# Performance work log

Measured on AMD Instinct MI355X. Metric: run time of the kernel, lower is better.

The kernel has to match this reference:

```python
import jax, jax.numpy as jnp
import numpy as np

B, S, E, H = 4, 2048, 1024, 16
D = E // H  # head_size = 64


def setup_inputs() -> dict:
    key = jax.random.key(0)
    k1, k2 = jax.random.split(key)
    x = jax.random.normal(k1, (B, S, E), dtype=jnp.float32)
    # fused QKV projection weight (torch Linear(E, 3E, bias=False))
    W_qkv = jax.random.normal(k2, (E, 3 * E), dtype=jnp.float32) * (1.0 / np.sqrt(E))
    return {"x": x, "W_qkv": W_qkv}


def reference(x, W_qkv):
    b, s, e = x.shape
    qkv = x @ W_qkv                              # [B,S,3E]
    q, k, v = jnp.split(qkv, 3, axis=-1)
    # [B,S,E] -> [B,H,S,D]
    q = q.reshape(b, s, H, D).transpose(0, 2, 1, 3)
    k = k.reshape(b, s, H, D).transpose(0, 2, 1, 3)
    v = v.reshape(b, s, H, D).transpose(0, 2, 1, 3)
    scores = jnp.einsum("bhqd,bhkd->bhqk", q, k) * (1.0 / np.sqrt(D))
    causal = jnp.tril(jnp.ones((s, s), dtype=bool))  # [S,S]
    scores = jnp.where(causal[None, None, :, :], scores, jnp.float32(-jnp.inf))
    attn = jax.nn.softmax(scores, axis=-1)
    # dropout is identity in eval mode (p effectively 0 for this baseline)
    out = jnp.einsum("bhqk,bhkd->bhqd", attn, v)  # [B,H,S,D]
    out = out.transpose(0, 2, 1, 3).reshape(b, s, e)
    # NOTE: original forward never applies output_projection; faithful omission.
    return out
```

## Files before the change

kernel.cpp:

```cpp
#include <hip/hip_runtime.h>
#include <hip/hip_bf16.h>
#include <cstdint>
#include <cstddef>

#define GLOBAL_AS __attribute__((address_space(1)))
#define LDS_AS __attribute__((address_space(3)))

typedef short bf16x8 __attribute__((ext_vector_type(8)));
typedef float f32x4 __attribute__((ext_vector_type(4)));

constexpr int Bq = 4, Sq = 2048, Eq = 1024, Hh = 16;
constexpr int M = Bq * Sq;
constexpr int K = 1024;
constexpr int N = 3 * Eq;

#define SMSC 0.18033688f
#define SMBIAS (-16.0f)

static __device__ __forceinline__ unsigned f2bf(float f) {
    union { float f; unsigned u; } v; v.f = f;
    unsigned r = v.u + 0x7fffu + ((v.u >> 16) & 1u);
    return r >> 16;
}

static __device__ __forceinline__ unsigned pk2(float a, float b) {
    union { __hip_bfloat162 h; unsigned u; } c;
    c.h = __float22bfloat162_rn(float2{a, b});
    return c.u;
}

__global__ __launch_bounds__(256) void prep(const float* __restrict__ X,
                                            unsigned short* __restrict__ Xb,
                                            const float* __restrict__ W,
                                            unsigned short* __restrict__ Wt) {
    __shared__ unsigned short tile[64 * 72];
    const int t = threadIdx.x;
    const int bx = blockIdx.x;
    if (bx < 4096) {
        size_t i = ((size_t)bx * 256 + t) * 8;
        float4 a = *reinterpret_cast<const float4*>(X + i);
        float4 b = *reinterpret_cast<const float4*>(X + i + 4);
        uint4 o;
        o.x = pk2(a.x, a.y);
        o.y = pk2(a.z, a.w);
        o.z = pk2(b.x, b.y);
        o.w = pk2(b.z, b.w);
        *reinterpret_cast<uint4*>(Xb + i) = o;
        return;
    }
    const int idx = bx - 4096;
    const int n0 = (idx % 48) * 64;
    const int k0 = (idx / 48) * 64;
    #pragma unroll
    for (int p = 0; p < 4; ++p) {
        int c = p * 256 + t;
        int row = c >> 4;
        int c4 = (c & 15) * 4;
        float4 v = *reinterpret_cast<const float4*>(W + (size_t)(k0 + row) * N + n0 + c4);
        *reinterpret_cast<unsigned*>(&tile[row * 72 + c4]) = pk2(v.x, v.y);
        *reinterpret_cast<unsigned*>(&tile[row * 72 + c4 + 2]) = pk2(v.z, v.w);
    }
    __syncthreads();
    #pragma unroll
    for (int p = 0; p < 2; ++p) {
        int c = t + p * 256;
        int n = c & 63;
        int kc = (c >> 6) * 8;
        unsigned v[8];
        #pragma unroll
        for (int j = 0; j < 8; ++j) v[j] = tile[(kc + j) * 72 + n];
        uint4 o;
        o.x = v[0] | (v[1] << 16);
        o.y = v[2] | (v[3] << 16);
        o.z = v[4] | (v[5] << 16);
        o.w = v[6] | (v[7] << 16);
        *reinterpret_cast<uint4*>(Wt + (size_t)(n0 + n) * K + k0 + kc) = o;
    }
}

__global__ __launch_bounds__(256) void gemm_qkv(const unsigned short* __restrict__ A,
                                                const unsigned short* __restrict__ Bt,
                                                unsigned short* __restrict__ C) {
    __shared__ unsigned short Alds[128 * 64];
    __shared__ unsigned short Blds[128 * 64];
    const int t = threadIdx.x;
    const int lane = t & 63, w = t >> 6;
    const int wm = w >> 1, wn = w & 1;
    const int m0 = blockIdx.y * 128, n0 = blockIdx.x * 128;
    const int lr = lane & 15, quad = lane >> 4;
    const int sw = lr & 7;

    f32x4 acc[4][4] = {};
    for (int k0 = 0; k0 < K; k0 += 64) {
        #pragma unroll
        for (int p = 0; p < 4; ++p) {
            int c = p * 256 + t;
            int row = c >> 3;
            int lch = (c & 7) ^ (row & 7);
            const unsigned short* ga = A + (size_t)(m0 + row) * K + k0 + lch * 8;
            __builtin_amdgcn_global_load_lds((const GLOBAL_AS unsigned int*)ga,
                                             (LDS_AS unsigned int*)&Alds[c * 8], 16, 0, 0);
            const unsigned short* gb = Bt + (size_t)(n0 + row) * K + k0 + lch * 8;
            __builtin_amdgcn_global_load_lds((const GLOBAL_AS unsigned int*)gb,
                                             (LDS_AS unsigned int*)&Blds[c * 8], 16, 0, 0);
        }
        __syncthreads();
        #pragma unroll
        for (int ks = 0; ks < 2; ++ks) {
            bf16x8 af[4], bfr[4];
            const int pch = ((ks * 4 + quad) ^ sw) << 3;
            #pragma unroll
            for (int mt = 0; mt < 4; ++mt)
                af[mt] = *reinterpret_cast<const bf16x8*>(
                    &Alds[(wm * 64 + mt * 16 + lr) * 64 + pch]);
            #pragma unroll
            for (int nt = 0; nt < 4; ++nt)
                bfr[nt] = *reinterpret_cast<const bf16x8*>(
                    &Blds[(wn * 64 + nt * 16 + lr) * 64 + pch]);
            #pragma unroll
            for (int mt = 0; mt < 4; ++mt)
                #pragma unroll
                for (int nt = 0; nt < 4; ++nt)
                    acc[mt][nt] = __builtin_amdgcn_mfma_f32_16x16x32_bf16(af[mt], bfr[nt],
                                                                          acc[mt][nt], 0, 0, 0);
        }
        __syncthreads();
    }
    #pragma unroll
    for (int mt = 0; mt < 4; ++mt)
        #pragma unroll
        for (int nt = 0; nt < 4; ++nt)
            #pragma unroll
            for (int r = 0; r < 4; ++r) {
                int row = m0 + wm * 64 + mt * 16 + quad * 4 + r;
                int col = n0 + wn * 64 + nt * 16 + lr;
                C[(size_t)row * N + col] = (unsigned short)f2bf(acc[mt][nt][r]);
            }
}

__global__ __launch_bounds__(256) void transpose_v(const unsigned short* __restrict__ QKV,
                                                   unsigned short* __restrict__ Vt) {
    __shared__ unsigned short tile[64 * 72];
    const int t = threadIdx.x;
    const int s0 = blockIdx.x * 64;
    const int h = blockIdx.y, b = blockIdx.z;
    #pragma unroll
    for (int p = 0; p < 2; ++p) {
        int c = t + p * 256;
        int row = c >> 3;
        int col0 = (c & 7) * 8;
        *reinterpret_cast<uint4*>(&tile[row * 72 + col0]) =
            *reinterpret_cast<const uint4*>(QKV + (size_t)(b * Sq + s0 + row) * N + 2 * Eq + h * 64 + col0);
    }
    __syncthreads();
    #pragma unroll
    for (int p = 0; p < 2; ++p) {
        int c = t + p * 256;
        int d = c & 63;
        int sc = (c >> 6) * 8;
        unsigned v[8];
        #pragma unroll
        for (int j = 0; j < 8; ++j) v[j] = tile[(sc + j) * 72 + d];
        uint4 o;
        o.x = v[0] | (v[1] << 16);
        o.y = v[2] | (v[3] << 16);
        o.z = v[4] | (v[5] << 16);
        o.w = v[6] | (v[7] << 16);
        *reinterpret_cast<uint4*>(Vt + (size_t)((b * Hh + h) * 64 + d) * Sq + s0 + sc) = o;
    }
}

__global__ __launch_bounds__(256) void flash_attn(const unsigned short* __restrict__ QKV,
                                                  const unsigned short* __restrict__ Vt,
                                                  float* __restrict__ Out) {
    __shared__ unsigned short Klds[2][64 * 64];
    __shared__ unsigned short Vlds[2][64 * 64];
    __shared__ unsigned short Plds[4][32 * 72];
    const int t = threadIdx.x;
    const int lane = t & 63, w = t >> 6;
    const int lr = lane & 15, quad = lane >> 4;
    const int hb = blockIdx.x;
    const int h = hb & 15, b = hb >> 4;
    const int i = 15 - (int)blockIdx.y;
    const int jmax = 2 * i + 1;
    const int jd = 2 * i + (w >> 1);
    const int qbase = i * 128 + w * 32;
    unsigned short* Pl = Plds[w];
    const int sw = lr & 7;

    const unsigned short* Kbase = QKV + (size_t)b * Sq * N + Eq + h * 64;
    const unsigned short* Vbase = Vt + (size_t)((b * Hh + h) * 64) * Sq;

    bf16x8 ones;
    #pragma unroll
    for (int z = 0; z < 8; ++z) ones[z] = (short)0x3F80;

    auto stage = [&](int j, int buf) {
        const int kv0 = j * 64;
        #pragma unroll
        for (int p = 0; p < 2; ++p) {
            int c = p * 256 + t;
            int row = c >> 3;
            int lch = (c & 7) ^ (row & 7);
            const unsigned short* gk = Kbase + (size_t)(kv0 + row) * N + lch * 8;
            __builtin_amdgcn_global_load_lds((const GLOBAL_AS unsigned int*)gk,
                                             (LDS_AS unsigned int*)&Klds[buf][c * 8], 16, 0, 0);
            const unsigned short* gv = Vbase + (size_t)row * Sq + kv0 + lch * 8;
            __builtin_amdgcn_global_load_lds((const GLOBAL_AS unsigned int*)gv,
                                             (LDS_AS unsigned int*)&Vlds[buf][c * 8], 16, 0, 0);
        }
    };

    bf16x8 qf[2][2];
    #pragma unroll
    for (int mt = 0; mt < 2; ++mt)
        #pragma unroll
        for (int ks = 0; ks < 2; ++ks)
            qf[mt][ks] = *reinterpret_cast<const bf16x8*>(
                QKV + (size_t)(b * Sq + qbase + mt * 16 + lr) * N + h * 64 + ks * 32 + quad * 8);

    f32x4 o[2][4] = {};
    f32x4 lsum[2] = {};

    stage(0, 0);
    int cur = 0;
    for (int j = 0; j <= jmax; ++j) {
        __syncthreads();
        if (j < jmax) stage(j + 1, cur ^ 1);

        if (j <= jd) {
            const unsigned short* Kb = Klds[cur];
            const unsigned short* Vb = Vlds[cur];
            const int kv0 = j * 64;

            f32x4 sa[2][4] = {};
            #pragma unroll
            for (int ks = 0; ks < 2; ++ks) {
                const int pch = ((ks * 4 + quad) ^ sw) << 3;
                #pragma unroll
                for (int nt = 0; nt < 4; ++nt) {
                    bf16x8 kf = *reinterpret_cast<const bf16x8*>(&Kb[(nt * 16 + lr) * 64 + pch]);
                    #pragma unroll
                    for (int mt = 0; mt < 2; ++mt)
                        sa[mt][nt] = __builtin_amdgcn_mfma_f32_16x16x32_bf16(qf[mt][ks], kf,
                                                                             sa[mt][nt], 0, 0, 0);
                }
            }

            if (j == jd) {
                #pragma unroll
                for (int mt = 0; mt < 2; ++mt)
                    #pragma unroll
                    for (int nt = 0; nt < 4; ++nt)
                        #pragma unroll
                        for (int r = 0; r < 4; ++r) {
                            int qg = qbase + mt * 16 + quad * 4 + r;
                            int kvg = kv0 + nt * 16 + lr;
                            float sc = fmaf(sa[mt][nt][r], SMSC, SMBIAS);
                            sc = (kvg > qg) ? -1e30f : sc;
                            Pl[(mt * 16 + quad * 4 + r) * 72 + nt * 16 + lr] =
                                (unsigned short)(__float_as_uint(exp2f(sc)) >> 16);
                        }
            } else {
                #pragma unroll
                for (int mt = 0; mt < 2; ++mt)
                    #pragma unroll
                    for (int nt = 0; nt < 4; ++nt)
                        #pragma unroll
                        for (int r = 0; r < 4; ++r)
                            Pl[(mt * 16 + quad * 4 + r) * 72 + nt * 16 + lr] =
                                (unsigned short)(__float_as_uint(
                                    exp2f(fmaf(sa[mt][nt][r], SMSC, SMBIAS))) >> 16);
            }
            asm volatile("s_waitcnt lgkmcnt(0)" ::: "memory");

            bf16x8 pf[2][2];
            #pragma unroll
            for (int mt = 0; mt < 2; ++mt)
                #pragma unroll
                for (int ks = 0; ks < 2; ++ks)
                    pf[mt][ks] = *reinterpret_cast<const bf16x8*>(
                        &Pl[(mt * 16 + lr) * 72 + ks * 32 + quad * 8]);

            #pragma unroll
            for (int ks = 0; ks < 2; ++ks) {
                const int pch = ((ks * 4 + quad) ^ sw) << 3;
                #pragma unroll
                for (int dt = 0; dt < 4; ++dt) {
                    bf16x8 vf = *reinterpret_cast<const bf16x8*>(&Vb[(dt * 16 + lr) * 64 + pch]);
                    #pragma unroll
                    for (int mt = 0; mt < 2; ++mt)
                        o[mt][dt] = __builtin_amdgcn_mfma_f32_16x16x32_bf16(pf[mt][ks], vf,
                                                                            o[mt][dt], 0, 0, 0);
                }
                #pragma unroll
                for (int mt = 0; mt < 2; ++mt)
                    lsum[mt] = __builtin_amdgcn_mfma_f32_16x16x32_bf16(pf[mt][ks], ones,
                                                                       lsum[mt], 0, 0, 0);
            }
        }
        cur ^= 1;
    }

    #pragma unroll
    for (int mt = 0; mt < 2; ++mt)
        #pragma unroll
        for (int r = 0; r < 4; ++r) {
            float inv = 1.0f / lsum[mt][r];
            int qg = qbase + mt * 16 + quad * 4 + r;
            #pragma unroll
            for (int dt = 0; dt < 4; ++dt)
                Out[(size_t)(b * Sq + qg) * Eq + h * 64 + dt * 16 + lr] = o[mt][dt][r] * inv;
        }
}

extern "C" void kernel_launch(void* const* d_in, const int* in_sizes, int n_in,
                              void* d_out, int out_size, void* d_ws, size_t ws_size,
                              hipStream_t stream) {
    const float* x  = (const float*)d_in[0];
    const float* Wq = (const float*)d_in[1];
    float* out = (float*)d_out;

    unsigned short* xb  = (unsigned short*)d_ws;
    unsigned short* qkv = xb + (size_t)M * K;
    unsigned short* Wt  = qkv + (size_t)M * N;
    unsigned short* Vt  = Wt + (size_t)N * K;

    prep<<<dim3(4096 + 768), 256, 0, stream>>>(x, xb, Wq, Wt);
    gemm_qkv<<<dim3(N / 128, M / 128), 256, 0, stream>>>(xb, Wt, qkv);
    transpose_v<<<dim3(Sq / 64, Hh, Bq), 256, 0, stream>>>(qkv, Vt);
    flash_attn<<<dim3(Hh * Bq, 16), 256, 0, stream>>>(qkv, Vt, out);
}
```

Before: 249.1 us.

## Fuse V transpose into GEMM epilogue and shrink attention KV tile to 32

The QKV GEMM epilogue now writes the V columns directly in transposed [B,H,D,S] layout, which removes the separate transpose_v kernel and its extra read and write of V. The flash attention kernel moves from 64-key to 32-key tiles with smaller LDS buffers and a launch-bounds occupancy hint of 4 blocks, so causal masking wastes less work per warp (each warp stops at its own diagonal tile). The cost is more loop iterations and barriers per block, and narrower uint2 scattered stores in the GEMM epilogue.

```diff
diff --git a/kernel.cpp b/kernel.cpp
--- a/kernel.cpp
+++ b/kernel.cpp
@@ -80,7 +80,8 @@
 
 __global__ __launch_bounds__(256) void gemm_qkv(const unsigned short* __restrict__ A,
                                                 const unsigned short* __restrict__ Bt,
-                                                unsigned short* __restrict__ C) {
+                                                unsigned short* __restrict__ C,
+                                                unsigned short* __restrict__ Vt) {
     __shared__ unsigned short Alds[128 * 64];
     __shared__ unsigned short Blds[128 * 64];
     const int t = threadIdx.x;
@@ -126,64 +127,49 @@
         }
         __syncthreads();
     }
-    #pragma unroll
-    for (int mt = 0; mt < 4; ++mt)
-        #pragma unroll
-        for (int nt = 0; nt < 4; ++nt)
-            #pragma unroll
-            for (int r = 0; r < 4; ++r) {
-                int row = m0 + wm * 64 + mt * 16 + quad * 4 + r;
-                int col = n0 + wn * 64 + nt * 16 + lr;
-                C[(size_t)row * N + col] = (unsigned short)f2bf(acc[mt][nt][r]);
+    if (n0 < 2 * Eq) {
+        #pragma unroll
+        for (int mt = 0; mt < 4; ++mt)
+            #pragma unroll
+            for (int nt = 0; nt < 4; ++nt)
+                #pragma unroll
+                for (int r = 0; r < 4; ++r) {
+                    int row = m0 + wm * 64 + mt * 16 + quad * 4 + r;
+                    int col = n0 + wn * 64 + nt * 16 + lr;
+                    C[(size_t)row * N + col] = (unsigned short)f2bf(acc[mt][nt][r]);
+                }
+    } else {
+        const int b2 = m0 >> 11;
+        const int sbase = (m0 & 2047) + wm * 64;
+        #pragma unroll
+        for (int mt = 0; mt < 4; ++mt)
+            #pragma unroll
+            for (int nt = 0; nt < 4; ++nt) {
+                int hd = n0 - 2 * Eq + wn * 64 + nt * 16 + lr;
+                size_t rowV = (size_t)(b2 * Hh + (hd >> 6)) * 64 + (hd & 63);
+                int s = sbase + mt * 16 + quad * 4;
+                uint2 val;
+                val.x = f2bf(acc[mt][nt][0]) | (f2bf(acc[mt][nt][1]) << 16);
+                val.y = f2bf(acc[mt][nt][2]) | (f2bf(acc[mt][nt][3]) << 16);
+                *reinterpret_cast<uint2*>(Vt + rowV * Sq + s) = val;
             }
-}
-
-__global__ __launch_bounds__(256) void transpose_v(const unsigned short* __restrict__ QKV,
-                                                   unsigned short* __restrict__ Vt) {
-    __shared__ unsigned short tile[64 * 72];
-    const int t = threadIdx.x;
-    const int s0 = blockIdx.x * 64;
-    const int h = blockIdx.y, b = blockIdx.z;
-    #pragma unroll
-    for (int p = 0; p < 2; ++p) {
-        int c = t + p * 256;
-        int row = c >> 3;
-        int col0 = (c & 7) * 8;
-        *reinterpret_cast<uint4*>(&tile[row * 72 + col0]) =
-            *reinterpret_cast<const uint4*>(QKV + (size_t)(b * Sq + s0 + row) * N + 2 * Eq + h * 64 + col0);
-    }
-    __syncthreads();
-    #pragma unroll
-    for (int p = 0; p < 2; ++p) {
-        int c = t + p * 256;
-        int d = c & 63;
-        int sc = (c >> 6) * 8;
-        unsigned v[8];
-        #pragma unroll
-        for (int j = 0; j < 8; ++j) v[j] = tile[(sc + j) * 72 + d];
-        uint4 o;
-        o.x = v[0] | (v[1] << 16);
-        o.y = v[2] | (v[3] << 16);
-        o.z = v[4] | (v[5] << 16);
-        o.w = v[6] | (v[7] << 16);
-        *reinterpret_cast<uint4*>(Vt + (size_t)((b * Hh + h) * 64 + d) * Sq + s0 + sc) = o;
-    }
-}
-
-__global__ __launch_bounds__(256) void flash_attn(const unsigned short* __restrict__ QKV,
-                                                  const unsigned short* __restrict__ Vt,
-                                                  float* __restrict__ Out) {
-    __shared__ unsigned short Klds[2][64 * 64];
-    __shared__ unsigned short Vlds[2][64 * 64];
-    __shared__ unsigned short Plds[4][32 * 72];
+    }
+}
+
+__global__ __launch_bounds__(256, 4) void flash_attn(const unsigned short* __restrict__ QKV,
+                                                     const unsigned short* __restrict__ Vt,
+                                                     float* __restrict__ Out) {
+    __shared__ unsigned short Klds[2][32 * 64];
+    __shared__ unsigned short Vlds[2][64 * 32];
+    __shared__ unsigned short Plds[4][32 * 40];
     const int t = threadIdx.x;
     const int lane = t & 63, w = t >> 6;
     const int lr = lane & 15, quad = lane >> 4;
     const int hb = blockIdx.x;
     const int h = hb & 15, b = hb >> 4;
     const int i = 15 - (int)blockIdx.y;
-    const int jmax = 2 * i + 1;
-    const int jd = 2 * i + (w >> 1);
+    const int jmax = 4 * i + 3;
+    const int jd = 4 * i + w;
     const int qbase = i * 128 + w * 32;
     unsigned short* Pl = Plds[w];
     const int sw = lr & 7;
@@ -196,18 +182,20 @@
     for (int z = 0; z < 8; ++z) ones[z] = (short)0x3F80;
 
     auto stage = [&](int j, int buf) {
-        const int kv0 = j * 64;
-        #pragma unroll
-        for (int p = 0; p < 2; ++p) {
-            int c = p * 256 + t;
-            int row = c >> 3;
-            int lch = (c & 7) ^ (row & 7);
+        const int kv0 = j * 32;
+        {
+            int row = t >> 3;
+            int lch = (t & 7) ^ (row & 7);
             const unsigned short* gk = Kbase + (size_t)(kv0 + row) * N + lch * 8;
             __builtin_amdgcn_global_load_lds((const GLOBAL_AS unsigned int*)gk,
-                                             (LDS_AS unsigned int*)&Klds[buf][c * 8], 16, 0, 0);
-            const unsigned short* gv = Vbase + (size_t)row * Sq + kv0 + lch * 8;
+                                             (LDS_AS unsigned int*)&Klds[buf][t * 8], 16, 0, 0);
+        }
+        {
+            int row = t >> 2;
+            int ch = t & 3;
+            const unsigned short* gv = Vbase + (size_t)row * Sq + kv0 + ch * 8;
             __builtin_amdgcn_global_load_lds((const GLOBAL_AS unsigned int*)gv,
-                                             (LDS_AS unsigned int*)&Vlds[buf][c * 8], 16, 0, 0);
+                                             (LDS_AS unsigned int*)&Vlds[buf][t * 8], 16, 0, 0);
         }
     };
 
@@ -231,14 +219,14 @@
         if (j <= jd) {
             const unsigned short* Kb = Klds[cur];
             const unsigned short* Vb = Vlds[cur];
-            const int kv0 = j * 64;
-
-            f32x4 sa[2][4] = {};
+            const int kv0 = j * 32;
+
+            f32x4 sa[2][2] = {};
             #pragma unroll
             for (int ks = 0; ks < 2; ++ks) {
                 const int pch = ((ks * 4 + quad) ^ sw) << 3;
                 #pragma unroll
-                for (int nt = 0; nt < 4; ++nt) {
+                for (int nt = 0; nt < 2; ++nt) {
                     bf16x8 kf = *reinterpret_cast<const bf16x8*>(&Kb[(nt * 16 + lr) * 64 + pch]);
                     #pragma unroll
                     for (int mt = 0; mt < 2; ++mt)
@@ -251,53 +239,46 @@
                 #pragma unroll
                 for (int mt = 0; mt < 2; ++mt)
                     #pragma unroll
-                    for (int nt = 0; nt < 4; ++nt)
+                    for (int nt = 0; nt < 2; ++nt)
                         #pragma unroll
                         for (int r = 0; r < 4; ++r) {
                             int qg = qbase + mt * 16 + quad * 4 + r;
                             int kvg = kv0 + nt * 16 + lr;
                             float sc = fmaf(sa[mt][nt][r], SMSC, SMBIAS);
                             sc = (kvg > qg) ? -1e30f : sc;
-                            Pl[(mt * 16 + quad * 4 + r) * 72 + nt * 16 + lr] =
+                            Pl[(mt * 16 + quad * 4 + r) * 40 + nt * 16 + lr] =
                                 (unsigned short)(__float_as_uint(exp2f(sc)) >> 16);
                         }
             } else {
                 #pragma unroll
                 for (int mt = 0; mt < 2; ++mt)
                     #pragma unroll
-                    for (int nt = 0; nt < 4; ++nt)
+                    for (int nt = 0; nt < 2; ++nt)
                         #pragma unroll
                         for (int r = 0; r < 4; ++r)
-                            Pl[(mt * 16 + quad * 4 + r) * 72 + nt * 16 + lr] =
+                            Pl[(mt * 16 + quad * 4 + r) * 40 + nt * 16 + lr] =
                                 (unsigned short)(__float_as_uint(
                                     exp2f(fmaf(sa[mt][nt][r], SMSC, SMBIAS))) >> 16);
             }
             asm volatile("s_waitcnt lgkmcnt(0)" ::: "memory");
 
-            bf16x8 pf[2][2];
+            bf16x8 pf[2];
             #pragma unroll
             for (int mt = 0; mt < 2; ++mt)
-                #pragma unroll
-                for (int ks = 0; ks < 2; ++ks)
-                    pf[mt][ks] = *reinterpret_cast<const bf16x8*>(
-                        &Pl[(mt * 16 + lr) * 72 + ks * 32 + quad * 8]);
-
-            #pragma unroll
-            for (int ks = 0; ks < 2; ++ks) {
-                const int pch = ((ks * 4 + quad) ^ sw) << 3;
-                #pragma unroll
-                for (int dt = 0; dt < 4; ++dt) {
-                    bf16x8 vf = *reinterpret_cast<const bf16x8*>(&Vb[(dt * 16 + lr) * 64 + pch]);
-                    #pragma unroll
-                    for (int mt = 0; mt < 2; ++mt)
-                        o[mt][dt] = __builtin_amdgcn_mfma_f32_16x16x32_bf16(pf[mt][ks], vf,
-                                                                            o[mt][dt], 0, 0, 0);
-                }
+                pf[mt] = *reinterpret_cast<const bf16x8*>(&Pl[(mt * 16 + lr) * 40 + quad * 8]);
+
+            #pragma unroll
+            for (int dt = 0; dt < 4; ++dt) {
+                bf16x8 vf = *reinterpret_cast<const bf16x8*>(&Vb[(dt * 16 + lr) * 32 + quad * 8]);
                 #pragma unroll
                 for (int mt = 0; mt < 2; ++mt)
-                    lsum[mt] = __builtin_amdgcn_mfma_f32_16x16x32_bf16(pf[mt][ks], ones,
-                                                                       lsum[mt], 0, 0, 0);
+                    o[mt][dt] = __builtin_amdgcn_mfma_f32_16x16x32_bf16(pf[mt], vf,
+                                                                        o[mt][dt], 0, 0, 0);
             }
+            #pragma unroll
+            for (int mt = 0; mt < 2; ++mt)
+                lsum[mt] = __builtin_amdgcn_mfma_f32_16x16x32_bf16(pf[mt], ones,
+                                                                   lsum[mt], 0, 0, 0);
         }
         cur ^= 1;
     }
@@ -327,7 +308,6 @@
     unsigned short* Vt  = Wt + (size_t)N * K;
 
     prep<<<dim3(4096 + 768), 256, 0, stream>>>(x, xb, Wq, Wt);
-    gemm_qkv<<<dim3(N / 128, M / 128), 256, 0, stream>>>(xb, Wt, qkv);
-    transpose_v<<<dim3(Sq / 64, Hh, Bq), 256, 0, stream>>>(qkv, Vt);
+    gemm_qkv<<<dim3(N / 128, M / 128), 256, 0, stream>>>(xb, Wt, qkv, Vt);
     flash_attn<<<dim3(Hh * Bq, 16), 256, 0, stream>>>(qkv, Vt, out);
 }
```

Result: faster. 228.4 us (-8.3%).
